# Kernel optimization log

Hardware: AMD Instinct MI355X
Metric: run time of the kernel (lower is better)

Reference implementation:

```python
import jax, jax.numpy as jnp
import numpy as np

N = 2048      # num nodes
F = 64        # in_channels
H = 16        # hidden_channels
O = 8         # out_channels


def setup_inputs() -> dict:
    key = jax.random.key(0)
    ks = jax.random.split(key, 16)
    s = 0.2  # small init scale
    inp = {
        "x": jax.random.normal(ks[0], (N, F), jnp.float32),
        "node_distances": jax.random.uniform(ks[1], (N, N), jnp.float32) * 5.0,
        "normalization": jax.random.uniform(ks[2], (N, N), jnp.float32) + 0.5,
        # per-feature f MLPs (1 -> H -> H -> O), stacked over features
        "fW1": jax.random.normal(ks[3], (F, H), jnp.float32) * s,
        "fb1": jnp.zeros((F, H), jnp.float32),
        "fW2": jax.random.normal(ks[4], (F, H, H), jnp.float32) * s,  # [F, out, in]
        "fb2": jnp.zeros((F, H), jnp.float32),
        "fW3": jax.random.normal(ks[5], (F, O, H), jnp.float32) * s,  # [F, out, in]
        "fb3": jnp.zeros((F, O), jnp.float32),
        # shared m MLP (1 -> H -> H -> 1), limited_m=True
        "mW1": jax.random.normal(ks[6], (H,), jnp.float32) * s,
        "mb1": jnp.zeros((H,), jnp.float32),
        "mW2": jax.random.normal(ks[7], (H, H), jnp.float32) * s,    # [out, in]
        "mb2": jnp.zeros((H,), jnp.float32),
        "mW3": jax.random.normal(ks[8], (H,), jnp.float32) * s,
        "mb3": jnp.zeros((), jnp.float32),
    }
    return inp


def reference(x, node_distances, normalization,
              fW1, fb1, fW2, fb2, fW3, fb3,
              mW1, mb1, mW2, mb2, mW3, mb3):
    # ---- per-feature f MLPs, vectorized over all nodes and features ----
    # x: [N, F] -> h: [N, F, H]
    h = jax.nn.relu(x[:, :, None] * fW1[None] + fb1[None])
    h = jax.nn.relu(jnp.einsum('nfh,fgh->nfg', h, fW2) + fb2[None])
    fx = jnp.einsum('nfh,foh->nfo', h, fW3) + fb3[None]        # [N, F, O]
    f_sums = fx.sum(axis=1)                                    # [N, O]

    # ---- m MLP applied elementwise to all pairwise distances ----
    d = node_distances                                         # [N, N]
    hm = jax.nn.relu(d[:, :, None] * mW1 + mb1)                # [N, N, H]
    hm = jax.nn.relu(jnp.einsum('ijh,gh->ijg', hm, mW2) + mb2)
    m_out = jnp.einsum('ijh,h->ij', hm, mW3) + mb3             # [N, N] (out dim 1)

    # normalize_m=True, m output dim == 1
    m_norm = m_out / normalization                             # [N, N]

    # pred[i] = sum_j m_norm[i, j] * f_sums[j]
    return m_norm @ f_sums                                     # [N, O]
```

## Files before the change

kernel.cpp:

```cpp
#include <hip/hip_runtime.h>

#define NN 2048
#define FF 64
#define HH 16
#define OO 8

#define BIGF  1e30f
#define BIGTH 1e29f
#define MAXBP 288
#define BPPAD 512
#define ABPAD 320
#define GCELL 1024

__device__ inline int cell_of(float d)
{
    int k = (int)floorf(fmaf(d, 32.f, 512.f));
    return min(max(k, 0), GCELL - 1);
}
__device__ inline int keycell(float v)
{
    return (v > BIGTH) ? GCELL : cell_of(v);
}

__device__ inline void l1_pattern(float c, const float* w1, const float* b1,
                                  float* a1, float* v1)
{
#pragma unroll
    for (int h = 0; h < HH; ++h) {
        const float arg = fmaf(w1[h], c, b1[h]);
        const bool act = arg > 0.f;
        a1[h] = act ? w1[h] : 0.f;
        v1[h] = act ? b1[h] : 0.f;
    }
}

__device__ inline void l2_arg(float c, int g,
                              const float* w1, const float* b1,
                              const float* w2, const float* b2,
                              float& A, float& B)
{
    float a1[HH], v1[HH];
    l1_pattern(c, w1, b1, a1, v1);
    float Aa = 0.f, Bb = b2[g];
#pragma unroll
    for (int h = 0; h < HH; ++h) {
        Aa = fmaf(w2[g * HH + h], a1[h], Aa);
        Bb = fmaf(w2[g * HH + h], v1[h], Bb);
    }
    A = Aa; B = Bb;
}

__device__ inline void pwl_coeffs(float c,
                                  const float* w1, const float* b1,
                                  const float* w2, const float* b2,
                                  const float* w3, float b3,
                                  float& alpha, float& beta)
{
    float a1[HH], v1[HH];
    l1_pattern(c, w1, b1, a1, v1);
    float al = 0.f, be = b3;
#pragma unroll
    for (int g = 0; g < HH; ++g) {
        float A = 0.f, B = b2[g];
#pragma unroll
        for (int h = 0; h < HH; ++h) {
            A = fmaf(w2[g * HH + h], a1[h], A);
            B = fmaf(w2[g * HH + h], v1[h], B);
        }
        const bool act = fmaf(A, c, B) > 0.f;
        al = fmaf(w3[g], act ? A : 0.f, al);
        be = fmaf(w3[g], act ? B : 0.f, be);
    }
    alpha = al; beta = be;
}

__device__ inline float seg_midpoint(float L, float R)
{
    float c;
    if (L <= -BIGTH && R >= BIGTH) c = 2.5f;
    else if (L <= -BIGTH)          c = R - 1.f;
    else if (R >= BIGTH)           c = L + 1.f;
    else                           c = 0.5f * (L + R);
    return fminf(fmaxf(c, -20.f), 20.f);
}

__global__ __launch_bounds__(512) void setup_kernel(
    const float* __restrict__ x,
    const float* __restrict__ fW1, const float* __restrict__ fb1,
    const float* __restrict__ fW2, const float* __restrict__ fb2,
    const float* __restrict__ fW3, const float* __restrict__ fb3,
    const float* __restrict__ mW1, const float* __restrict__ mb1,
    const float* __restrict__ mW2, const float* __restrict__ mb2,
    const float* __restrict__ mW3, const float* __restrict__ mb3,
    float* __restrict__ part,
    float* __restrict__ bp_out, float* __restrict__ ab_out,
    float* __restrict__ cell4_out, float* __restrict__ cellb_out)
{
    const int tid = threadIdx.x;

    if (blockIdx.x < 256) {
        __shared__ float sw1[HH], sb1[HH], sw2[HH * HH], sb2[HH], sw3[OO * HH], sb3[OO];
        const int f = blockIdx.x & 63;

        if (tid < HH) {
            sw1[tid] = fW1[f * HH + tid];
            sb1[tid] = fb1[f * HH + tid];
            sb2[tid] = fb2[f * HH + tid];
        }
        if (tid < HH * HH) sw2[tid] = fW2[f * HH * HH + tid];
        if (tid < OO * HH) sw3[tid] = fW3[f * OO * HH + tid];
        if (tid < OO)      sb3[tid] = fb3[f * OO + tid];
        __syncthreads();

        const int n = (blockIdx.x >> 6) * 512 + tid;
        const float xv = x[n * FF + f];

        float h1[HH];
#pragma unroll
        for (int h = 0; h < HH; ++h)
            h1[h] = fmaxf(fmaf(xv, sw1[h], sb1[h]), 0.f);

        float h2[HH];
#pragma unroll
        for (int g = 0; g < HH; ++g) {
            float a = sb2[g];
#pragma unroll
            for (int h = 0; h < HH; ++h) a = fmaf(sw2[g * HH + h], h1[h], a);
            h2[g] = fmaxf(a, 0.f);
        }

#pragma unroll
        for (int o = 0; o < OO; ++o) {
            float a = sb3[o];
#pragma unroll
            for (int h = 0; h < HH; ++h) a = fmaf(sw3[o * HH + h], h2[h], a);
            part[(n * FF + f) * OO + o] = a;
        }
        return;
    }

    __shared__ float w1[HH], b1[HH], w2[HH * HH], b2[HH], w3[HH];
    __shared__ float b3s;
    __shared__ float ends[18];
    __shared__ float cand[MAXBP];
    __shared__ float sorted[BPPAD];
    __shared__ float t16s[HH];
    __shared__ float sal[ABPAD], sbe[ABPAD];

    if (tid < HH) { w1[tid] = mW1[tid]; b1[tid] = mb1[tid]; b2[tid] = mb2[tid]; w3[tid] = mW3[tid]; }
    if (tid < HH * HH) w2[tid] = mW2[tid];
    if (tid == 0) b3s = mb3[0];
    sorted[tid] = BIGF;
    __syncthreads();

    if (tid < HH) {
        const float w = w1[tid];
        const float t = -b1[tid] / w;
        cand[tid] = (w != 0.f && t > -10.f && t < 10.f) ? t : BIGF;
    }
    __syncthreads();
    if (tid < HH) {
        const float my = cand[tid];
        int r = 0;
        for (int k = 0; k < HH; ++k) {
            const float o = cand[k];
            r += (o < my) || (o == my && k < tid);
        }
        t16s[r] = my;
    }
    __syncthreads();
    if (tid == 0)  ends[0] = -BIGF;
    if (tid < HH)  ends[tid + 1] = t16s[tid];
    if (tid == 0)  ends[17] = BIGF;
    __syncthreads();

    if (tid < 17 * HH) {
        const int iv = tid >> 4;
        const int g  = tid & 15;
        const float L = ends[iv], R = ends[iv + 1];
        float xx = BIGF;
        if (L < BIGTH) {
            const float c = seg_midpoint(L, R);
            float A, B;
            l2_arg(c, g, w1, b1, w2, b2, A, B);
            const float t = -B / A;
            if (t > L && t < R && t > -10.f && t < 10.f) xx = t;
        }
        cand[HH + tid] = xx;
    }
    __syncthreads();

    if (tid < MAXBP) {
        const float my = cand[tid];
        int r = 0;
        for (int k = 0; k < MAXBP; ++k) {
            const float o = cand[k];
            r += (o < my) || (o == my && k < tid);
        }
        sorted[r] = my;
    }
    __syncthreads();

    bp_out[tid] = sorted[tid];

    if (tid < ABPAD) {
        float al = 0.f, be = 0.f;
        if (tid <= MAXBP) {
            const float L = (tid == 0)    ? -BIGF : sorted[tid - 1];
            const float R = (tid < MAXBP) ? sorted[tid] : BIGF;
            const float c = seg_midpoint(L, R);
            pwl_coeffs(c, w1, b1, w2, b2, w3, b3s, al, be);
        }
        sal[tid] = al; sbe[tid] = be;
        ab_out[tid] = al;
        ab_out[ABPAD + tid] = be;
    }
    __syncthreads();

    for (int k = tid; k < GCELL; k += 512) {
        int base = 0, nxt = 0;
#pragma unroll
        for (int st = 256; st >= 1; st >>= 1) {
            base += (keycell(sorted[base + st - 1]) < k)     ? st : 0;
            nxt  += (keycell(sorted[nxt  + st - 1]) < k + 1) ? st : 0;
        }
        const int cnt = nxt - base;
        float4 r; float bk;
        if (cnt == 0) {
            r.x = sal[base]; r.y = sbe[base]; r.z = r.x; r.w = r.y;
            bk = -BIGF;
        } else {
            const float bmin = sorted[base];
            const float bmax = sorted[nxt - 1];
            if (bmin == bmax) {
                r.x = sal[base];       r.y = sbe[base];
                r.z = sal[base + cnt]; r.w = sbe[base + cnt];
                bk = bmin;
            } else {
                r.x = r.y = r.z = r.w = 0.f;
                bk = __int_as_float(0x7fc00000);
            }
        }
        reinterpret_cast<float4*>(cell4_out)[k] = r;
        cellb_out[k] = bk;
    }
}

__global__ __launch_bounds__(256) void fsum_reduce(
    const float* __restrict__ part, float* __restrict__ f_sums)
{
    const int n = blockIdx.x * 4 + (threadIdx.x >> 6);
    const int f = threadIdx.x & 63;
    const float4* p = reinterpret_cast<const float4*>(part + (n * FF + f) * OO);
    float4 a = p[0];
    float4 b = p[1];
#pragma unroll
    for (int off = 32; off > 0; off >>= 1) {
        a.x += __shfl_down(a.x, off, 64);
        a.y += __shfl_down(a.y, off, 64);
        a.z += __shfl_down(a.z, off, 64);
        a.w += __shfl_down(a.w, off, 64);
        b.x += __shfl_down(b.x, off, 64);
        b.y += __shfl_down(b.y, off, 64);
        b.z += __shfl_down(b.z, off, 64);
        b.w += __shfl_down(b.w, off, 64);
    }
    if (f == 0) {
        float4* q = reinterpret_cast<float4*>(f_sums + n * OO);
        q[0] = a;
        q[1] = b;
    }
}

__global__ __launch_bounds__(256) void mnet_kernel(
    const float* __restrict__ d, const float* __restrict__ norm,
    const float* __restrict__ f_sums,
    const float* __restrict__ bp_g, const float* __restrict__ ab_g,
    const float* __restrict__ cell4_g, const float* __restrict__ cellb_g,
    float* __restrict__ out)
{
    __shared__ float red[4][OO];
    const int tid = threadIdx.x;
    const int i = blockIdx.x;

    const float* drow = d + (size_t)i * NN;
    const float* nrow = norm + (size_t)i * NN;
    const float4* c4 = reinterpret_cast<const float4*>(cell4_g);

    float acc[OO];
#pragma unroll
    for (int o = 0; o < OO; ++o) acc[o] = 0.f;

#pragma unroll
    for (int it = 0; it < 2; ++it) {
        const int j0 = (it * 256 + tid) * 4;
        const float4 dv4 = *reinterpret_cast<const float4*>(drow + j0);
        const float4 nv4 = *reinterpret_cast<const float4*>(nrow + j0);
        float4 fs[8];
#pragma unroll
        for (int e = 0; e < 4; ++e) {
            fs[2 * e]     = *reinterpret_cast<const float4*>(f_sums + (j0 + e) * OO);
            fs[2 * e + 1] = *reinterpret_cast<const float4*>(f_sums + (j0 + e) * OO + 4);
        }
        const float dvs[4] = {dv4.x, dv4.y, dv4.z, dv4.w};
        const float nvs[4] = {nv4.x, nv4.y, nv4.z, nv4.w};
#pragma unroll
        for (int e = 0; e < 4; ++e) {
            const float dv = dvs[e];
            const int k = cell_of(dv);
            const float4 r = c4[k];
            const float bk = cellb_g[k];
            float al = (dv < bk) ? r.x : r.z;
            float be = (dv < bk) ? r.y : r.w;
            if (bk != bk) {
                int lo = 0;
#pragma unroll
                for (int st = 256; st >= 1; st >>= 1)
                    lo += (bp_g[lo + st - 1] <= dv) ? st : 0;
                al = ab_g[lo]; be = ab_g[ABPAD + lo];
            }
            const float mn = fmaf(al, dv, be) * __builtin_amdgcn_rcpf(nvs[e]);
            acc[0] = fmaf(mn, fs[2 * e].x, acc[0]);
            acc[1] = fmaf(mn, fs[2 * e].y, acc[1]);
            acc[2] = fmaf(mn, fs[2 * e].z, acc[2]);
            acc[3] = fmaf(mn, fs[2 * e].w, acc[3]);
            acc[4] = fmaf(mn, fs[2 * e + 1].x, acc[4]);
            acc[5] = fmaf(mn, fs[2 * e + 1].y, acc[5]);
            acc[6] = fmaf(mn, fs[2 * e + 1].z, acc[6]);
            acc[7] = fmaf(mn, fs[2 * e + 1].w, acc[7]);
        }
    }

#pragma unroll
    for (int off = 32; off > 0; off >>= 1) {
#pragma unroll
        for (int o = 0; o < OO; ++o) acc[o] += __shfl_down(acc[o], off, 64);
    }
    const int wave = tid >> 6;
    const int lane = tid & 63;
    if (lane == 0) {
#pragma unroll
        for (int o = 0; o < OO; ++o) red[wave][o] = acc[o];
    }
    __syncthreads();
    if (tid == 0) {
#pragma unroll
        for (int o = 0; o < OO; ++o)
            out[i * OO + o] = red[0][o] + red[1][o] + red[2][o] + red[3][o];
    }
}

extern "C" void kernel_launch(void* const* d_in, const int* in_sizes, int n_in,
                              void* d_out, int out_size, void* d_ws, size_t ws_size,
                              hipStream_t stream)
{
    const float* x   = (const float*)d_in[0];
    const float* nd  = (const float*)d_in[1];
    const float* nm  = (const float*)d_in[2];
    const float* fW1 = (const float*)d_in[3];
    const float* fb1 = (const float*)d_in[4];
    const float* fW2 = (const float*)d_in[5];
    const float* fb2 = (const float*)d_in[6];
    const float* fW3 = (const float*)d_in[7];
    const float* fb3 = (const float*)d_in[8];
    const float* mW1 = (const float*)d_in[9];
    const float* mb1 = (const float*)d_in[10];
    const float* mW2 = (const float*)d_in[11];
    const float* mb2 = (const float*)d_in[12];
    const float* mW3 = (const float*)d_in[13];
    const float* mb3 = (const float*)d_in[14];
    float* out = (float*)d_out;

    float* part   = (float*)d_ws;
    float* f_sums = part + (size_t)NN * FF * OO;
    float* bp     = f_sums + (size_t)NN * OO;
    float* ab     = bp + BPPAD;
    float* cell4  = ab + 2 * ABPAD;
    float* cellb  = cell4 + 4 * GCELL;

    setup_kernel<<<257, 512, 0, stream>>>(
        x, fW1, fb1, fW2, fb2, fW3, fb3,
        mW1, mb1, mW2, mb2, mW3, mb3,
        part, bp, ab, cell4, cellb);
    fsum_reduce<<<512, 256, 0, stream>>>(part, f_sums);
    mnet_kernel<<<NN, 256, 0, stream>>>(nd, nm, f_sums, bp, ab, cell4, cellb, out);
}
```

Baseline: 49.70 us.

## Parallelize breakpoint cell table across blocks and transpose f_sums layout

Drops the serial sort of breakpoints and the per-segment coefficient table inside one setup block. Instead four blocks each build part of the 1024-cell lookup directly, scanning the unsorted candidate list per cell and evaluating the piecewise-linear coefficients at cell-local midpoints. The rare mixed-cell fallback in the main kernel now does a linear scan over the candidates and recomputes coefficients. Separately, f_sums is stored transposed ([O][N]) so the main kernel loads it with coalesced float4 reads. The intent is to shorten the serial setup tail and improve memory access in mnet, at the cost of redundant per-cell scans and a slower fallback path.

Result: no change. 50.19 us (+1.0%).

```diff
diff --git a/kernel.cpp b/kernel.cpp
--- a/kernel.cpp
+++ b/kernel.cpp
@@ -8,8 +8,7 @@
 #define BIGF  1e30f
 #define BIGTH 1e29f
 #define MAXBP 288
-#define BPPAD 512
-#define ABPAD 320
+#define CANDPAD 320
 #define GCELL 1024
 
 __device__ inline int cell_of(float d)
@@ -93,7 +92,7 @@
     const float* __restrict__ mW2, const float* __restrict__ mb2,
     const float* __restrict__ mW3, const float* __restrict__ mb3,
     float* __restrict__ part,
-    float* __restrict__ bp_out, float* __restrict__ ab_out,
+    float* __restrict__ cand_g,
     float* __restrict__ cell4_out, float* __restrict__ cellb_out)
 {
     const int tid = threadIdx.x;
@@ -143,14 +142,11 @@
     __shared__ float b3s;
     __shared__ float ends[18];
     __shared__ float cand[MAXBP];
-    __shared__ float sorted[BPPAD];
     __shared__ float t16s[HH];
-    __shared__ float sal[ABPAD], sbe[ABPAD];
 
     if (tid < HH) { w1[tid] = mW1[tid]; b1[tid] = mb1[tid]; b2[tid] = mb2[tid]; w3[tid] = mW3[tid]; }
     if (tid < HH * HH) w2[tid] = mW2[tid];
     if (tid == 0) b3s = mb3[0];
-    sorted[tid] = BIGF;
     __syncthreads();
 
     if (tid < HH) {
@@ -190,64 +186,39 @@
     }
     __syncthreads();
 
-    if (tid < MAXBP) {
-        const float my = cand[tid];
-        int r = 0;
-        for (int k = 0; k < MAXBP; ++k) {
-            const float o = cand[k];
-            r += (o < my) || (o == my && k < tid);
-        }
-        sorted[r] = my;
-    }
-    __syncthreads();
-
-    bp_out[tid] = sorted[tid];
-
-    if (tid < ABPAD) {
-        float al = 0.f, be = 0.f;
-        if (tid <= MAXBP) {
-            const float L = (tid == 0)    ? -BIGF : sorted[tid - 1];
-            const float R = (tid < MAXBP) ? sorted[tid] : BIGF;
-            const float c = seg_midpoint(L, R);
-            pwl_coeffs(c, w1, b1, w2, b2, w3, b3s, al, be);
-        }
-        sal[tid] = al; sbe[tid] = be;
-        ab_out[tid] = al;
-        ab_out[ABPAD + tid] = be;
-    }
-    __syncthreads();
-
-    for (int k = tid; k < GCELL; k += 512) {
-        int base = 0, nxt = 0;
-#pragma unroll
-        for (int st = 256; st >= 1; st >>= 1) {
-            base += (keycell(sorted[base + st - 1]) < k)     ? st : 0;
-            nxt  += (keycell(sorted[nxt  + st - 1]) < k + 1) ? st : 0;
-        }
-        const int cnt = nxt - base;
-        float4 r; float bk;
-        if (cnt == 0) {
-            r.x = sal[base]; r.y = sbe[base]; r.z = r.x; r.w = r.y;
-            bk = -BIGF;
-        } else {
-            const float bmin = sorted[base];
-            const float bmax = sorted[nxt - 1];
-            if (bmin == bmax) {
-                r.x = sal[base];       r.y = sbe[base];
-                r.z = sal[base + cnt]; r.w = sbe[base + cnt];
-                bk = bmin;
-            } else {
-                r.x = r.y = r.z = r.w = 0.f;
-                bk = __int_as_float(0x7fc00000);
-            }
-        }
-        reinterpret_cast<float4*>(cell4_out)[k] = r;
-        cellb_out[k] = bk;
-    }
+    if (blockIdx.x == 256 && tid < CANDPAD)
+        cand_g[tid] = (tid < MAXBP) ? cand[tid] : BIGF;
+
+    const int cell  = (blockIdx.x - 256) * 256 + (tid >> 1);
+    const int which = tid & 1;
+
+    int cnt = 0; float bmin = BIGF, bmax = -BIGF;
+    for (int k = 0; k < MAXBP; ++k) {
+        const float v = cand[k];
+        if (keycell(v) == cell) { ++cnt; bmin = fminf(bmin, v); bmax = fmaxf(bmax, v); }
+    }
+
+    const float cl = (float)(cell - 512) * 0.03125f;
+    const float cr = cl + 0.03125f;
+
+    float al = 0.f, be = 0.f, bk;
+    if (cnt == 0) {
+        pwl_coeffs(0.5f * (cl + cr), w1, b1, w2, b2, w3, b3s, al, be);
+        bk = -BIGF;
+    } else if (bmin == bmax) {
+        const float c = which ? 0.5f * (bmin + cr) : 0.5f * (cl + bmin);
+        pwl_coeffs(c, w1, b1, w2, b2, w3, b3s, al, be);
+        bk = bmin;
+    } else {
+        bk = __int_as_float(0x7fc00000);
+    }
+    cell4_out[cell * 4 + which * 2 + 0] = al;
+    cell4_out[cell * 4 + which * 2 + 1] = be;
+    if (which == 0) cellb_out[cell] = bk;
 }
 
 __global__ __launch_bounds__(256) void fsum_reduce(
-    const float* __restrict__ part, float* __restrict__ f_sums)
+    const float* __restrict__ part, float* __restrict__ fsT)
 {
     const int n = blockIdx.x * 4 + (threadIdx.x >> 6);
     const int f = threadIdx.x & 63;
@@ -266,17 +237,25 @@
         b.w += __shfl_down(b.w, off, 64);
     }
     if (f == 0) {
-        float4* q = reinterpret_cast<float4*>(f_sums + n * OO);
-        q[0] = a;
-        q[1] = b;
+        fsT[0 * NN + n] = a.x;
+        fsT[1 * NN + n] = a.y;
+        fsT[2 * NN + n] = a.z;
+        fsT[3 * NN + n] = a.w;
+        fsT[4 * NN + n] = b.x;
+        fsT[5 * NN + n] = b.y;
+        fsT[6 * NN + n] = b.z;
+        fsT[7 * NN + n] = b.w;
     }
 }
 
 __global__ __launch_bounds__(256) void mnet_kernel(
     const float* __restrict__ d, const float* __restrict__ norm,
-    const float* __restrict__ f_sums,
-    const float* __restrict__ bp_g, const float* __restrict__ ab_g,
+    const float* __restrict__ fsT,
+    const float* __restrict__ cand_g,
     const float* __restrict__ cell4_g, const float* __restrict__ cellb_g,
+    const float* __restrict__ mW1, const float* __restrict__ mb1,
+    const float* __restrict__ mW2, const float* __restrict__ mb2,
+    const float* __restrict__ mW3, const float* __restrict__ mb3,
     float* __restrict__ out)
 {
     __shared__ float red[4][OO];
@@ -296,12 +275,11 @@
         const int j0 = (it * 256 + tid) * 4;
         const float4 dv4 = *reinterpret_cast<const float4*>(drow + j0);
         const float4 nv4 = *reinterpret_cast<const float4*>(nrow + j0);
-        float4 fs[8];
-#pragma unroll
-        for (int e = 0; e < 4; ++e) {
-            fs[2 * e]     = *reinterpret_cast<const float4*>(f_sums + (j0 + e) * OO);
-            fs[2 * e + 1] = *reinterpret_cast<const float4*>(f_sums + (j0 + e) * OO + 4);
-        }
+        float4 fo[OO];
+#pragma unroll
+        for (int o = 0; o < OO; ++o)
+            fo[o] = *reinterpret_cast<const float4*>(fsT + (size_t)o * NN + j0);
+
         const float dvs[4] = {dv4.x, dv4.y, dv4.z, dv4.w};
         const float nvs[4] = {nv4.x, nv4.y, nv4.z, nv4.w};
 #pragma unroll
@@ -313,21 +291,24 @@
             float al = (dv < bk) ? r.x : r.z;
             float be = (dv < bk) ? r.y : r.w;
             if (bk != bk) {
-                int lo = 0;
-#pragma unroll
-                for (int st = 256; st >= 1; st >>= 1)
-                    lo += (bp_g[lo + st - 1] <= dv) ? st : 0;
-                al = ab_g[lo]; be = ab_g[ABPAD + lo];
+                float lower = -BIGF, upper = BIGF;
+                for (int kk = 0; kk < MAXBP; ++kk) {
+                    const float v = cand_g[kk];
+                    if (v <= dv) lower = fmaxf(lower, v);
+                    else         upper = fminf(upper, v);
+                }
+                pwl_coeffs(seg_midpoint(lower, upper),
+                           mW1, mb1, mW2, mb2, mW3, mb3[0], al, be);
             }
             const float mn = fmaf(al, dv, be) * __builtin_amdgcn_rcpf(nvs[e]);
-            acc[0] = fmaf(mn, fs[2 * e].x, acc[0]);
-            acc[1] = fmaf(mn, fs[2 * e].y, acc[1]);
-            acc[2] = fmaf(mn, fs[2 * e].z, acc[2]);
-            acc[3] = fmaf(mn, fs[2 * e].w, acc[3]);
-            acc[4] = fmaf(mn, fs[2 * e + 1].x, acc[4]);
-            acc[5] = fmaf(mn, fs[2 * e + 1].y, acc[5]);
-            acc[6] = fmaf(mn, fs[2 * e + 1].z, acc[6]);
-            acc[7] = fmaf(mn, fs[2 * e + 1].w, acc[7]);
+            acc[0] = fmaf(mn, (&fo[0].x)[e], acc[0]);
+            acc[1] = fmaf(mn, (&fo[1].x)[e], acc[1]);
+            acc[2] = fmaf(mn, (&fo[2].x)[e], acc[2]);
+            acc[3] = fmaf(mn, (&fo[3].x)[e], acc[3]);
+            acc[4] = fmaf(mn, (&fo[4].x)[e], acc[4]);
+            acc[5] = fmaf(mn, (&fo[5].x)[e], acc[5]);
+            acc[6] = fmaf(mn, (&fo[6].x)[e], acc[6]);
+            acc[7] = fmaf(mn, (&fo[7].x)[e], acc[7]);
         }
     }
 
@@ -371,17 +352,17 @@
     const float* mb3 = (const float*)d_in[14];
     float* out = (float*)d_out;
 
-    float* part   = (float*)d_ws;
-    float* f_sums = part + (size_t)NN * FF * OO;
-    float* bp     = f_sums + (size_t)NN * OO;
-    float* ab     = bp + BPPAD;
-    float* cell4  = ab + 2 * ABPAD;
-    float* cellb  = cell4 + 4 * GCELL;
-
-    setup_kernel<<<257, 512, 0, stream>>>(
+    float* part  = (float*)d_ws;
+    float* fsT   = part + (size_t)NN * FF * OO;
+    float* candg = fsT + (size_t)OO * NN;
+    float* cell4 = candg + CANDPAD;
+    float* cellb = cell4 + 4 * GCELL;
+
+    setup_kernel<<<260, 512, 0, stream>>>(
         x, fW1, fb1, fW2, fb2, fW3, fb3,
         mW1, mb1, mW2, mb2, mW3, mb3,
-        part, bp, ab, cell4, cellb);
-    fsum_reduce<<<512, 256, 0, stream>>>(part, f_sums);
-    mnet_kernel<<<NN, 256, 0, stream>>>(nd, nm, f_sums, bp, ab, cell4, cellb, out);
-}
+        part, candg, cell4, cellb);
+    fsum_reduce<<<512, 256, 0, stream>>>(part, fsT);
+    mnet_kernel<<<NN, 256, 0, stream>>>(nd, nm, fsT, candg, cell4, cellb,
+                                        mW1, mb1, mW2, mb2, mW3, mb3, out);
+}
```
